# Optimization experiments

Hardware: AMD Instinct MI355X
Metric: run time of the kernel (lower is better)

Reference implementation:

```python
import jax, jax.numpy as jnp
import numpy as np

THRESH = 1e-4


def setup_inputs() -> dict:
    key = jax.random.key(0)
    B, C, H, W = 16, 1, 1024, 1024
    u = jax.random.uniform(key, (B, C, H, W), dtype=jnp.float32)
    batch_mask = (u < 0.1).astype(jnp.float32)
    # fixed discrete-Laplacian stencil hardcoded in the module's __init__
    kernel = jnp.array([[0.0, -0.25, 0.0],
                        [-0.25, 1.0, -0.25],
                        [0.0, -0.25, 0.0]], dtype=jnp.float32)
    weight = kernel[None, None, :, :]  # OIHW = [1,1,3,3]
    return {"batch_mask": batch_mask, "weight": weight, "iter_num": 5}


def reference(batch_mask, weight, iter_num):
    def body(_, m):
        # ReplicationPad2d(1) == edge padding
        p = jnp.pad(m, ((0, 0), (0, 0), (1, 1), (1, 1)), mode="edge")
        res = jax.lax.conv_general_dilated(
            p, weight, window_strides=(1, 1), padding="VALID",
            dimension_numbers=("NCHW", "OIHW", "NCHW"))
        # batch_mask[res.abs() > 1e-4] = 1.0
        return jnp.where(jnp.abs(res) > THRESH, jnp.float32(1.0), m)

    return jax.lax.fori_loop(0, iter_num, body, batch_mask)
```

## Files before the change

### kernel.cpp

```cpp
#include <hip/hip_runtime.h>
#include <stdint.h>


#define IMG_H 1024
#define IMG_W 1024
#define WORDS 16
#define TR    16
#define HALO  5
#define LR    (TR + 2*HALO)

typedef float vfloat4 __attribute__((ext_vector_type(4)));

__global__ __launch_bounds__(256) void dilate_mask_kernel(
    const float* __restrict__ in, float* __restrict__ out)
{
    __shared__ uint64_t bufA[LR][WORDS];
    __shared__ uint64_t bufB[LR][WORDS];

    const int tile = blockIdx.x;
    const int img  = blockIdx.y;
    const int tid  = threadIdx.x;
    const int lane = tid & 63;
    const int wave = tid >> 6;
    const int rowBase = tile * TR;

    const float* imgIn  = in  + (size_t)img * IMG_H * IMG_W;
    float*       imgOut = out + (size_t)img * IMG_H * IMG_W;

    for (int r = wave; r < LR; r += 4) {
        const int irow = rowBase - HALO + r;
        uint64_t myword = 0ull;
        if (irow >= 0 && irow < IMG_H) {
            const float* rowPtr = imgIn + (size_t)irow * IMG_W;
            #pragma unroll
            for (int w = 0; w < WORDS; ++w) {
                const float v = rowPtr[w * 64 + lane];
                const uint64_t b = __ballot(v != 0.f);
                if (lane == w) myword = b;
            }
        }
        if (lane < WORDS) bufA[r][lane] = myword;
    }
    __syncthreads();

    uint64_t (*src)[WORDS] = bufA;
    uint64_t (*dst)[WORDS] = bufB;
    #pragma unroll
    for (int it = 0; it < 5; ++it) {
        for (int idx = tid; idx < LR * WORDS; idx += 256) {
            const int r = idx >> 4;
            const int w = idx & 15;
            const uint64_t cur = src[r][w];
            const uint64_t lft = (w > 0)         ? src[r][w - 1] : 0ull;
            const uint64_t rgt = (w < WORDS - 1) ? src[r][w + 1] : 0ull;
            const uint64_t up  = (r > 0)         ? src[r - 1][w] : 0ull;
            const uint64_t dn  = (r < LR - 1)    ? src[r + 1][w] : 0ull;
            dst[r][w] = cur | (cur << 1) | (lft >> 63)
                            | (cur >> 1) | (rgt << 63)
                            | up | dn;
        }
        __syncthreads();
        uint64_t (*tmp)[WORDS] = src; src = dst; dst = tmp;
    }

    for (int rr = wave; rr < TR; rr += 4) {
        const int r = HALO + rr;
        vfloat4* rowPtr = (vfloat4*)(imgOut + (size_t)(rowBase + rr) * IMG_W);
        #pragma unroll
        for (int seg = 0; seg < 4; ++seg) {
            const uint64_t word = src[r][seg * 4 + (lane >> 4)];
            const uint32_t nib = (uint32_t)(word >> (4 * (lane & 15))) & 0xFu;
            vfloat4 o;
            o.x = (nib & 1u) ? 1.f : 0.f;
            o.y = (nib & 2u) ? 1.f : 0.f;
            o.z = (nib & 4u) ? 1.f : 0.f;
            o.w = (nib & 8u) ? 1.f : 0.f;
            __builtin_nontemporal_store(o, &rowPtr[seg * 64 + lane]);
        }
    }
}

extern "C" void kernel_launch(void* const* d_in, const int* in_sizes, int n_in,
                              void* d_out, int out_size, void* d_ws, size_t ws_size,
                              hipStream_t stream)
{
    const float* batch_mask = (const float*)d_in[0];
    float* out = (float*)d_out;

    dim3 grid(IMG_H / TR, 16);
    dim3 block(256);
    hipLaunchKernelGGL(dilate_mask_kernel, grid, block, 0, stream, batch_mask, out);
}
```

Measured before the change: 115.1 us.

## Replace iterative bit-packed dilation with closed-form diamond dilation via horizontal prefixes

Swaps five iterated 4-neighbour dilation passes, each followed by a barrier, for a direct diamond-shaped (L1 radius 5) dilation. It precomputes horizontal dilations of radius 0..5 per row, then ORs row r±d dilated by 5-d. This cuts the sweeps over the shared bit buffer and the syncthreads calls, but uses more shared memory for the six horizontal-radius buffers. The image-boundary behaviour (zero-padding in bit space) is unchanged from the previous version.

```diff
diff --git a/kernel.cpp b/kernel.cpp
--- a/kernel.cpp
+++ b/kernel.cpp
@@ -14,8 +14,8 @@
 __global__ __launch_bounds__(256) void dilate_mask_kernel(
     const float* __restrict__ in, float* __restrict__ out)
 {
-    __shared__ uint64_t bufA[LR][WORDS];
-    __shared__ uint64_t bufB[LR][WORDS];
+    __shared__ uint64_t sH[HALO + 1][LR][WORDS];
+    __shared__ uint64_t sOut[TR][WORDS];
 
     const int tile = blockIdx.x;
     const int img  = blockIdx.y;
@@ -39,36 +39,43 @@
                 if (lane == w) myword = b;
             }
         }
-        if (lane < WORDS) bufA[r][lane] = myword;
+        if (lane < WORDS) sH[0][r][lane] = myword;
     }
     __syncthreads();
 
-    uint64_t (*src)[WORDS] = bufA;
-    uint64_t (*dst)[WORDS] = bufB;
-    #pragma unroll
-    for (int it = 0; it < 5; ++it) {
-        for (int idx = tid; idx < LR * WORDS; idx += 256) {
-            const int r = idx >> 4;
-            const int w = idx & 15;
-            const uint64_t cur = src[r][w];
-            const uint64_t lft = (w > 0)         ? src[r][w - 1] : 0ull;
-            const uint64_t rgt = (w < WORDS - 1) ? src[r][w + 1] : 0ull;
-            const uint64_t up  = (r > 0)         ? src[r - 1][w] : 0ull;
-            const uint64_t dn  = (r < LR - 1)    ? src[r + 1][w] : 0ull;
-            dst[r][w] = cur | (cur << 1) | (lft >> 63)
-                            | (cur >> 1) | (rgt << 63)
-                            | up | dn;
+    for (int idx = tid; idx < LR * WORDS; idx += 256) {
+        const int r = idx >> 4;
+        const int w = idx & 15;
+        const uint64_t cur = sH[0][r][w];
+        const uint64_t lft = (w > 0)         ? sH[0][r][w - 1] : 0ull;
+        const uint64_t rgt = (w < WORDS - 1) ? sH[0][r][w + 1] : 0ull;
+        uint64_t h = cur;
+        #pragma unroll
+        for (int k = 1; k <= HALO; ++k) {
+            h |= (cur << k) | (lft >> (64 - k))
+               | (cur >> k) | (rgt << (64 - k));
+            sH[k][r][w] = h;
         }
-        __syncthreads();
-        uint64_t (*tmp)[WORDS] = src; src = dst; dst = tmp;
     }
+    __syncthreads();
+
+    for (int idx = tid; idx < TR * WORDS; idx += 256) {
+        const int rr = idx >> 4;
+        const int w  = idx & 15;
+        const int r  = rr + HALO;
+        uint64_t acc = sH[HALO][r][w];
+        #pragma unroll
+        for (int d = 1; d <= HALO; ++d)
+            acc |= sH[HALO - d][r - d][w] | sH[HALO - d][r + d][w];
+        sOut[rr][w] = acc;
+    }
+    __syncthreads();
 
     for (int rr = wave; rr < TR; rr += 4) {
-        const int r = HALO + rr;
         vfloat4* rowPtr = (vfloat4*)(imgOut + (size_t)(rowBase + rr) * IMG_W);
         #pragma unroll
         for (int seg = 0; seg < 4; ++seg) {
-            const uint64_t word = src[r][seg * 4 + (lane >> 4)];
+            const uint64_t word = sOut[rr][seg * 4 + (lane >> 4)];
             const uint32_t nib = (uint32_t)(word >> (4 * (lane & 15))) & 0xFu;
             vfloat4 o;
             o.x = (nib & 1u) ? 1.f : 0.f;
```

Result: no change. 113.6 us (-1.3%).
